# Kernel optimization log

Hardware: AMD Instinct MI355X
Metric: run time of the kernel (lower is better)

The kernel has to match this reference:

```python
import jax, jax.numpy as jnp
import numpy as np

N = 100000   # nodes
E = 1600000  # edges (edge_index1)
F_IN = 53    # num_features_xd
D1 = 128     # output_dim1
D2 = 64      # output_dim2
G = 512      # graphs in batch


def setup_inputs() -> dict:
    key = jax.random.key(0)
    ks = jax.random.split(key, 16)
    kaiming = lambda k, fi, fo: jax.random.normal(k, (fi, fo), jnp.float32) * np.float32(np.sqrt(2.0 / fi))
    glorot = lambda k, fi, fo: jax.random.normal(k, (fi, fo), jnp.float32) * np.float32(np.sqrt(1.0 / fi))
    return {
        "x": jax.random.normal(ks[0], (N, F_IN), jnp.float32),
        "edge_inter": jax.random.randint(ks[1], (2, E), 0, N),
        "edge_intra": jax.random.randint(ks[2], (2, E), 0, N),
        "batch": jnp.sort(jax.random.randint(ks[3], (N,), 0, G)),
        "num_graphs": G,
        "w1": kaiming(ks[4], F_IN, D1), "b1": jnp.zeros((D1,), jnp.float32),
        "w2": kaiming(ks[5], D1, D2), "b2": jnp.zeros((D2,), jnp.float32),
        "gat_w": glorot(ks[6], D2, D2),
        "att_src": jax.random.normal(ks[7], (D2,), jnp.float32) * 0.1,
        "att_dst": jax.random.normal(ks[8], (D2,), jnp.float32) * 0.1,
        "gat_b": jnp.zeros((D2,), jnp.float32),
        "gcn_w": glorot(ks[9], D2, 2 * D2), "gcn_b": jnp.zeros((2 * D2,), jnp.float32),
        "fc1_w": glorot(ks[10], 2 * D2, 512), "fc1_b": jnp.zeros((512,), jnp.float32),
        "fc2_w": glorot(ks[11], 512, 256), "fc2_b": jnp.zeros((256,), jnp.float32),
        "out_w": glorot(ks[12], 256, 1), "out_b": jnp.zeros((1,), jnp.float32),
    }


def reference(x, edge_inter, edge_intra, batch, num_graphs,
              w1, b1, w2, b2, gat_w, att_src, att_dst, gat_b,
              gcn_w, gcn_b, fc1_w, fc1_b, fc2_w, fc2_b, out_w, out_b):
    n = x.shape[0]
    # node_embed: two dense layers + relu
    h = jax.nn.relu(x @ w1 + b1)
    h = jax.nn.relu(h @ w2 + b2)

    # add self-loops (PyG default for GATConv and GCNConv)
    loops = jnp.arange(n)
    src = jnp.concatenate([edge_inter[0], loops])  # message source j
    dst = jnp.concatenate([edge_inter[1], loops])  # message target i

    # ---- GATConv (heads=1): gather -> score -> edge softmax -> scatter ----
    hp = h @ gat_w                           # [N, D2]
    a_s = hp @ att_src                       # [N]
    a_d = hp @ att_dst                       # [N]
    e = jax.nn.leaky_relu(a_s[src] + a_d[dst], negative_slope=0.2)  # [E+N]
    emax = jax.ops.segment_max(e, dst, num_segments=n)
    ee = jnp.exp(e - emax[dst])
    denom = jax.ops.segment_sum(ee, dst, num_segments=n)
    alpha = ee / denom[dst]                  # edge softmax per target node
    h = jax.ops.segment_sum(alpha[:, None] * hp[src], dst, num_segments=n) + gat_b
    h = jax.nn.relu(h)

    # ---- GCNConv: symmetric-normalized sparse aggregation ----
    hw = h @ gcn_w                           # [N, 2*D2]
    deg = jax.ops.segment_sum(jnp.ones_like(e), dst, num_segments=n)
    d_inv = jnp.where(deg > 0, deg ** -0.5, 0.0)
    norm = d_inv[src] * d_inv[dst]           # [E+N]
    h = jax.ops.segment_sum(norm[:, None] * hw[src], dst, num_segments=n) + gcn_b
    h = jax.nn.relu(h)

    # ---- global max pool over graphs ----
    g = jax.ops.segment_max(h, batch, num_segments=num_graphs)
    g = jnp.maximum(g, 0.0)  # guard empty segments (-inf); h >= 0 after relu

    # ---- MLP head (dropout is identity in eval mode) ----
    z = jax.nn.relu(g @ fc1_w + fc1_b)
    z = jax.nn.relu(z @ fc2_w + fc2_b)
    return z @ out_w + out_b
```

## Files before the change

kernel.cpp:

```cpp
#include <hip/hip_runtime.h>
#include <hip/hip_bf16.h>

#define F_IN 53
#define D1   128
#define D2   64
#define D3   128
#define H1SZ 512
#define H2SZ 256

#define BUKSZ   256
#define BUKMAX  512
#define CAP     5120
#define PART_CH 4096

__global__ void k_vecproj(const float* __restrict__ gat_w,
                          const float* __restrict__ att_src,
                          const float* __restrict__ att_dst,
                          float* __restrict__ v_src, float* __restrict__ v_dst) {
    int k = threadIdx.x;
    float as = 0.f, ad = 0.f;
    #pragma unroll
    for (int c = 0; c < D2; ++c) {
        float w = gat_w[k * D2 + c];
        as = fmaf(w, att_src[c], as);
        ad = fmaf(w, att_dst[c], ad);
    }
    v_src[k] = as;
    v_dst[k] = ad;
}

__global__ __launch_bounds__(256) void k_fused(const float* __restrict__ x,
                                               const float* __restrict__ w1,
                                               const float* __restrict__ b1,
                                               const float* __restrict__ w2,
                                               const float* __restrict__ b2,
                                               const float* __restrict__ gat_w,
                                               const float* __restrict__ v_src,
                                               const float* __restrict__ v_dst,
                                               float* __restrict__ hp,
                                               float* __restrict__ a_s,
                                               float* __restrict__ a_d,
                                               const int* __restrict__ ei,
                                               int* __restrict__ gcount,
                                               int2* __restrict__ tmp,
                                               const int* __restrict__ batch,
                                               int* __restrict__ gstart,
                                               int N, int E, int NBUK, int G,
                                               int embB, int partB) {
    __shared__ __align__(16) union {
        struct { float buf[32][64]; float h1s[32][D1]; } e;
        int hist[BUKMAX];
    } sm;
    int tid = threadIdx.x;
    int bid = blockIdx.x;

    if (bid >= embB) {
        if (bid < embB + partB) {
            for (int i = tid; i < NBUK; i += 256) sm.hist[i] = 0;
            __syncthreads();
            int k0 = (bid - embB) * PART_CH;
            int ss[16], dd[16];
            #pragma unroll
            for (int i = 0; i < 16; ++i) {
                int k = k0 + i * 256 + tid;
                if (k < E) {
                    ss[i] = ei[k];
                    dd[i] = ei[E + k];
                    atomicAdd(&sm.hist[dd[i] >> 8], 1);
                } else {
                    dd[i] = -1;
                }
            }
            __syncthreads();
            for (int b = tid; b < NBUK; b += 256) {
                int c = sm.hist[b];
                if (c > 0) sm.hist[b] = b * CAP + atomicAdd(&gcount[b], c);
            }
            __syncthreads();
            #pragma unroll
            for (int i = 0; i < 16; ++i) {
                if (dd[i] >= 0) {
                    int b = dd[i] >> 8;
                    int pos = atomicAdd(&sm.hist[b], 1);
                    if (pos < (b + 1) * CAP) tmp[pos] = make_int2(ss[i], dd[i]);
                }
            }
        } else {
            int n = (bid - embB - partB) * 256 + tid;
            if (n < N) {
                int b = batch[n];
                if (n == 0) {
                    for (int g = 0; g <= b; ++g) gstart[g] = 0;
                } else {
                    int pb = batch[n - 1];
                    for (int g = pb + 1; g <= b; ++g) gstart[g] = n;
                }
                if (n == N - 1) {
                    for (int g = b + 1; g <= G; ++g) gstart[g] = N;
                }
            }
        }
        return;
    }

    int n0 = bid * 32;
    for (int i = tid; i < 32 * F_IN; i += 256) {
        int node = i / F_IN, kk = i - node * F_IN;
        sm.e.buf[node][kk] = x[(size_t)n0 * F_IN + i];
    }
    __syncthreads();
    int c = tid & 63, grp = tid >> 6;
    int nb = grp * 8;
    {
        float acc0[8], acc1[8];
        float bb0 = b1[c], bb1 = b1[c + 64];
        #pragma unroll
        for (int j = 0; j < 8; ++j) { acc0[j] = bb0; acc1[j] = bb1; }
        #pragma unroll 1
        for (int kc = 0; kc < 13; ++kc) {
            int k4 = kc * 4;
            float wa0 = w1[(k4 + 0) * D1 + c];
            float wa1 = w1[(k4 + 1) * D1 + c];
            float wa2 = w1[(k4 + 2) * D1 + c];
            float wa3 = w1[(k4 + 3) * D1 + c];
            float wb0 = w1[(k4 + 0) * D1 + c + 64];
            float wb1 = w1[(k4 + 1) * D1 + c + 64];
            float wb2 = w1[(k4 + 2) * D1 + c + 64];
            float wb3 = w1[(k4 + 3) * D1 + c + 64];
            #pragma unroll
            for (int j = 0; j < 8; ++j) {
                float4 xv = *reinterpret_cast<const float4*>(&sm.e.buf[nb + j][k4]);
                acc0[j] = fmaf(xv.x, wa0, acc0[j]);
                acc0[j] = fmaf(xv.y, wa1, acc0[j]);
                acc0[j] = fmaf(xv.z, wa2, acc0[j]);
                acc0[j] = fmaf(xv.w, wa3, acc0[j]);
                acc1[j] = fmaf(xv.x, wb0, acc1[j]);
                acc1[j] = fmaf(xv.y, wb1, acc1[j]);
                acc1[j] = fmaf(xv.z, wb2, acc1[j]);
                acc1[j] = fmaf(xv.w, wb3, acc1[j]);
            }
        }
        {
            float wa = w1[52 * D1 + c], wb = w1[52 * D1 + c + 64];
            #pragma unroll
            for (int j = 0; j < 8; ++j) {
                float xv = sm.e.buf[nb + j][52];
                acc0[j] = fmaf(xv, wa, acc0[j]);
                acc1[j] = fmaf(xv, wb, acc1[j]);
            }
        }
        #pragma unroll
        for (int j = 0; j < 8; ++j) {
            sm.e.h1s[nb + j][c]      = fmaxf(acc0[j], 0.f);
            sm.e.h1s[nb + j][c + 64] = fmaxf(acc1[j], 0.f);
        }
    }
    float h2v[8];
    {
        float bb = b2[c];
        #pragma unroll
        for (int j = 0; j < 8; ++j) h2v[j] = bb;
        #pragma unroll 1
        for (int kc = 0; kc < 32; ++kc) {
            int k4 = kc * 4;
            float w0 = w2[(k4 + 0) * D2 + c];
            float w1v = w2[(k4 + 1) * D2 + c];
            float w2v = w2[(k4 + 2) * D2 + c];
            float w3v = w2[(k4 + 3) * D2 + c];
            #pragma unroll
            for (int j = 0; j < 8; ++j) {
                float4 hv = *reinterpret_cast<const float4*>(&sm.e.h1s[nb + j][k4]);
                h2v[j] = fmaf(hv.x, w0, h2v[j]);
                h2v[j] = fmaf(hv.y, w1v, h2v[j]);
                h2v[j] = fmaf(hv.z, w2v, h2v[j]);
                h2v[j] = fmaf(hv.w, w3v, h2v[j]);
            }
        }
        #pragma unroll
        for (int j = 0; j < 8; ++j) {
            float v = fmaxf(h2v[j], 0.f);
            h2v[j] = v;
            sm.e.buf[nb + j][c] = v;
        }
    }
    {
        float vs = v_src[c], vd = v_dst[c];
        #pragma unroll
        for (int j = 0; j < 8; ++j) {
            float ps = h2v[j] * vs, pd = h2v[j] * vd;
            #pragma unroll
            for (int off = 32; off; off >>= 1) {
                ps += __shfl_down(ps, off);
                pd += __shfl_down(pd, off);
            }
            if (c == 0) { int n = n0 + nb + j; a_s[n] = ps; a_d[n] = pd; }
        }
    }
    {
        float acc[8];
        #pragma unroll
        for (int j = 0; j < 8; ++j) acc[j] = 0.f;
        #pragma unroll 1
        for (int kc = 0; kc < 16; ++kc) {
            int k4 = kc * 4;
            float w0 = gat_w[(k4 + 0) * D2 + c];
            float w1v = gat_w[(k4 + 1) * D2 + c];
            float w2v = gat_w[(k4 + 2) * D2 + c];
            float w3v = gat_w[(k4 + 3) * D2 + c];
            #pragma unroll
            for (int j = 0; j < 8; ++j) {
                float4 hv = *reinterpret_cast<const float4*>(&sm.e.buf[nb + j][k4]);
                acc[j] = fmaf(hv.x, w0, acc[j]);
                acc[j] = fmaf(hv.y, w1v, acc[j]);
                acc[j] = fmaf(hv.z, w2v, acc[j]);
                acc[j] = fmaf(hv.w, w3v, acc[j]);
            }
        }
        #pragma unroll
        for (int j = 0; j < 8; ++j)
            hp[(size_t)(n0 + nb + j) * D2 + c] = acc[j];
    }
}

__global__ __launch_bounds__(256) void k_build(const int2* __restrict__ tmp,
                                               const int* __restrict__ gcount,
                                               int* __restrict__ offs,
                                               int* __restrict__ degi,
                                               float* __restrict__ dinv,
                                               int* __restrict__ csr_src, int N) {
    __shared__ int ldeg[256];
    __shared__ int lsc[256];
    __shared__ int lcur[256];
    __shared__ int pref[256];
    int tid = threadIdx.x;
    int b = blockIdx.x;
    int n0 = b * BUKSZ;
    int nvalid = min(BUKSZ, N - n0);
    int cnt = min(gcount[b], CAP);
    int acc = 0;
    for (int i = tid; i < b; i += 256) acc += min(gcount[i], CAP);
    pref[tid] = acc;
    ldeg[tid] = 0;
    __syncthreads();
    #pragma unroll
    for (int off = 128; off; off >>= 1) {
        if (tid < off) pref[tid] += pref[tid + off];
        __syncthreads();
    }
    int base = pref[0] + n0;
    for (int i = tid; i < cnt; i += 256) {
        int2 e = tmp[b * CAP + i];
        atomicAdd(&ldeg[e.y & 255], 1);
    }
    __syncthreads();
    int d = (tid < nvalid) ? (ldeg[tid] + 1) : 0;
    lsc[tid] = d;
    __syncthreads();
    #pragma unroll
    for (int off = 1; off < 256; off <<= 1) {
        int u = (tid >= off) ? lsc[tid - off] : 0;
        __syncthreads();
        lsc[tid] += u;
        __syncthreads();
    }
    int excl = lsc[tid] - d;
    if (tid < nvalid) {
        int n = n0 + tid;
        offs[n] = base + excl;
        degi[n] = d;
        dinv[n] = rsqrtf((float)d);
        lcur[tid] = excl;
    }
    __syncthreads();
    for (int i = tid; i < cnt; i += 256) {
        int2 e = tmp[b * CAP + i];
        int nl = e.y & 255;
        int r = atomicAdd(&lcur[nl], 1);
        csr_src[base + r] = e.x;
    }
    __syncthreads();
    if (tid < nvalid) {
        int r = atomicAdd(&lcur[tid], 1);
        csr_src[base + r] = n0 + tid;
    }
}

__global__ __launch_bounds__(256) void k_gat(const int* __restrict__ csr_src,
                                             const int* __restrict__ offs,
                                             const int* __restrict__ degi,
                                             const float* __restrict__ a_s,
                                             const float* __restrict__ a_d,
                                             const float* __restrict__ hp,
                                             const float* __restrict__ gat_b,
                                             const float* __restrict__ dinv,
                                             float* __restrict__ hscaled, int N) {
    __shared__ float ac[4][128];
    __shared__ int   si[4][128];
    int wv = threadIdx.x >> 6, lane = threadIdx.x & 63;
    int node = blockIdx.x * 4 + wv;
    if (node >= N) return;
    int start = offs[node], deg = degi[node];
    int dcap = min(deg, 128);
    float adn = a_d[node];
    float m = -1e30f, ssum = 0.f;
    for (int p = lane; p < deg; p += 64) {
        int s = csr_src[start + p];
        float e = a_s[s] + adn;
        e = (e > 0.f) ? e : 0.2f * e;
        if (p < 128) { ac[wv][p] = e; si[wv][p] = s; }
        float mn = fmaxf(m, e);
        ssum = ssum * __expf(m - mn) + __expf(e - mn);
        m = mn;
    }
    #pragma unroll
    for (int off = 32; off; off >>= 1) {
        float om = __shfl_xor(m, off);
        float os = __shfl_xor(ssum, off);
        float mn = fmaxf(m, om);
        ssum = ssum * __expf(m - mn) + os * __expf(om - mn);
        m = mn;
    }
    float rinv = 1.0f / ssum;
    if (lane < dcap)      ac[wv][lane]      = __expf(ac[wv][lane] - m) * rinv;
    if (lane + 64 < dcap) ac[wv][lane + 64] = __expf(ac[wv][lane + 64] - m) * rinv;
    float acc = 0.f;
    for (int pp = 0; pp < dcap; pp += 16) {
        int s[16]; float w[16];
        #pragma unroll
        for (int i = 0; i < 16; ++i) {
            int q = pp + i;
            int qc = (q < dcap) ? q : (dcap - 1);
            s[i] = si[wv][qc];
            w[i] = (q < dcap) ? ac[wv][q] : 0.f;
        }
        float v[16];
        #pragma unroll
        for (int i = 0; i < 16; ++i) v[i] = hp[(size_t)s[i] * D2 + lane];
        #pragma unroll
        for (int i = 0; i < 16; ++i) acc = fmaf(w[i], v[i], acc);
    }
    for (int p = 128; p < deg; ++p) {
        int s = csr_src[start + p];
        float e = a_s[s] + adn;
        e = (e > 0.f) ? e : 0.2f * e;
        acc = fmaf(__expf(e - m) * rinv, hp[(size_t)s * D2 + lane], acc);
    }
    hscaled[(size_t)node * D2 + lane] = dinv[node] * fmaxf(acc + gat_b[lane], 0.f);
}

__global__ __launch_bounds__(256) void k_gcn(const int* __restrict__ csr_src,
                                             const int* __restrict__ offs,
                                             const int* __restrict__ degi,
                                             const float* __restrict__ dinv,
                                             const float* __restrict__ hscaled,
                                             float* __restrict__ hagg, int N) {
    int node = blockIdx.x * 4 + (threadIdx.x >> 6);
    int lane = threadIdx.x & 63;
    if (node >= N) return;
    int start = offs[node], deg = degi[node];
    float acc = 0.f;
    for (int pp = 0; pp < deg; pp += 16) {
        int s[16];
        #pragma unroll
        for (int i = 0; i < 16; ++i) {
            int q = pp + i;
            int qc = (q < deg) ? q : (deg - 1);
            s[i] = csr_src[start + qc];
        }
        float v[16];
        #pragma unroll
        for (int i = 0; i < 16; ++i) v[i] = hscaled[(size_t)s[i] * D2 + lane];
        #pragma unroll
        for (int i = 0; i < 16; ++i) acc += (pp + i < deg) ? v[i] : 0.f;
    }
    hagg[(size_t)node * D2 + lane] = acc * dinv[node];
}

__global__ __launch_bounds__(512) void k_pool(const float* __restrict__ hagg,
                                              const float* __restrict__ gcn_w,
                                              const float* __restrict__ gcn_b,
                                              const int* __restrict__ gstart,
                                              float* __restrict__ g) {
    __shared__ float ws[D2 * D3];
    __shared__ __align__(16) float rows[16 * D2];
    __shared__ float red[512];
    int tid = threadIdx.x;
    int gi = blockIdx.x;
    for (int i = tid; i < D2 * D3; i += 512) ws[i] = gcn_w[i];
    int ns = gstart[gi], ne = gstart[gi + 1];
    int col = tid & 127, grp = tid >> 7;
    float bias = gcn_b[col];
    float runmax = 0.f;
    for (int base = ns; base < ne; base += 16) {
        int cnt = min(16, ne - base);
        __syncthreads();
        for (int i = tid; i < cnt * D2; i += 512)
            rows[i] = hagg[(size_t)base * D2 + i];
        __syncthreads();
        int nb = grp * 4;
        float a0 = bias, a1 = bias, a2 = bias, a3 = bias;
        #pragma unroll 4
        for (int kc = 0; kc < 16; ++kc) {
            int k4 = kc * 4;
            float w0 = ws[(k4 + 0) * D3 + col];
            float w1v = ws[(k4 + 1) * D3 + col];
            float w2v = ws[(k4 + 2) * D3 + col];
            float w3v = ws[(k4 + 3) * D3 + col];
            float4 r0 = *reinterpret_cast<const float4*>(&rows[(nb + 0) * D2 + k4]);
            float4 r1 = *reinterpret_cast<const float4*>(&rows[(nb + 1) * D2 + k4]);
            float4 r2 = *reinterpret_cast<const float4*>(&rows[(nb + 2) * D2 + k4]);
            float4 r3 = *reinterpret_cast<const float4*>(&rows[(nb + 3) * D2 + k4]);
            a0 = fmaf(r0.x, w0, a0); a0 = fmaf(r0.y, w1v, a0);
            a0 = fmaf(r0.z, w2v, a0); a0 = fmaf(r0.w, w3v, a0);
            a1 = fmaf(r1.x, w0, a1); a1 = fmaf(r1.y, w1v, a1);
            a1 = fmaf(r1.z, w2v, a1); a1 = fmaf(r1.w, w3v, a1);
            a2 = fmaf(r2.x, w0, a2); a2 = fmaf(r2.y, w1v, a2);
            a2 = fmaf(r2.z, w2v, a2); a2 = fmaf(r2.w, w3v, a2);
            a3 = fmaf(r3.x, w0, a3); a3 = fmaf(r3.y, w1v, a3);
            a3 = fmaf(r3.z, w2v, a3); a3 = fmaf(r3.w, w3v, a3);
        }
        if (nb + 0 < cnt) runmax = fmaxf(runmax, a0);
        if (nb + 1 < cnt) runmax = fmaxf(runmax, a1);
        if (nb + 2 < cnt) runmax = fmaxf(runmax, a2);
        if (nb + 3 < cnt) runmax = fmaxf(runmax, a3);
    }
    red[tid] = runmax;
    __syncthreads();
    if (tid < 128) {
        float v = fmaxf(fmaxf(red[tid], red[tid + 128]),
                        fmaxf(red[tid + 256], red[tid + 384]));
        g[(size_t)gi * D3 + tid] = v;
    }
}

__global__ __launch_bounds__(512) void k_fc1(const float* __restrict__ g,
                                             const float* __restrict__ w,
                                             const float* __restrict__ b,
                                             float* __restrict__ z1) {
    __shared__ float gs[4 * D3];
    int t = threadIdx.x;
    int g0 = blockIdx.x * 4;
    if (t < 4 * D3) gs[t] = g[(size_t)g0 * D3 + t];
    __syncthreads();
    float bias = b[t];
    float a0 = bias, a1 = bias, a2 = bias, a3 = bias;
    for (int k = 0; k < D3; ++k) {
        float wv = w[k * H1SZ + t];
        a0 = fmaf(gs[k], wv, a0);
        a1 = fmaf(gs[D3 + k], wv, a1);
        a2 = fmaf(gs[2 * D3 + k], wv, a2);
        a3 = fmaf(gs[3 * D3 + k], wv, a3);
    }
    z1[(size_t)(g0 + 0) * H1SZ + t] = fmaxf(a0, 0.f);
    z1[(size_t)(g0 + 1) * H1SZ + t] = fmaxf(a1, 0.f);
    z1[(size_t)(g0 + 2) * H1SZ + t] = fmaxf(a2, 0.f);
    z1[(size_t)(g0 + 3) * H1SZ + t] = fmaxf(a3, 0.f);
}

__global__ __launch_bounds__(256) void k_fc2(const float* __restrict__ z1,
                                             const float* __restrict__ w,
                                             const float* __restrict__ b,
                                             float* __restrict__ z2) {
    __shared__ float zs[4 * H1SZ];
    int t = threadIdx.x;
    int g0 = blockIdx.x * 4;
    for (int i = t; i < 4 * H1SZ; i += 256) zs[i] = z1[(size_t)g0 * H1SZ + i];
    __syncthreads();
    float bias = b[t];
    float a0 = bias, a1 = bias, a2 = bias, a3 = bias;
    for (int k = 0; k < H1SZ; ++k) {
        float wv = w[k * H2SZ + t];
        a0 = fmaf(zs[k], wv, a0);
        a1 = fmaf(zs[H1SZ + k], wv, a1);
        a2 = fmaf(zs[2 * H1SZ + k], wv, a2);
        a3 = fmaf(zs[3 * H1SZ + k], wv, a3);
    }
    z2[(size_t)(g0 + 0) * H2SZ + t] = fmaxf(a0, 0.f);
    z2[(size_t)(g0 + 1) * H2SZ + t] = fmaxf(a1, 0.f);
    z2[(size_t)(g0 + 2) * H2SZ + t] = fmaxf(a2, 0.f);
    z2[(size_t)(g0 + 3) * H2SZ + t] = fmaxf(a3, 0.f);
}

__global__ __launch_bounds__(256) void k_out(const float* __restrict__ z2,
                                             const float* __restrict__ out_w,
                                             const float* __restrict__ out_b,
                                             float* __restrict__ out) {
    __shared__ float red[4];
    int gi = blockIdx.x, t = threadIdx.x;
    float p = z2[(size_t)gi * H2SZ + t] * out_w[t];
    #pragma unroll
    for (int off = 32; off; off >>= 1) p += __shfl_down(p, off);
    int lane = t & 63, w = t >> 6;
    if (lane == 0) red[w] = p;
    __syncthreads();
    if (t == 0) out[gi] = red[0] + red[1] + red[2] + red[3] + out_b[0];
}

extern "C" void kernel_launch(void* const* d_in, const int* in_sizes, int n_in,
                              void* d_out, int out_size, void* d_ws, size_t ws_size,
                              hipStream_t stream) {
    const float* x        = (const float*)d_in[0];
    const int*   ei       = (const int*)d_in[1];
    const int*   batch    = (const int*)d_in[3];
    const float* w1       = (const float*)d_in[5];
    const float* b1       = (const float*)d_in[6];
    const float* w2       = (const float*)d_in[7];
    const float* b2       = (const float*)d_in[8];
    const float* gat_w    = (const float*)d_in[9];
    const float* att_src  = (const float*)d_in[10];
    const float* att_dst  = (const float*)d_in[11];
    const float* gat_b    = (const float*)d_in[12];
    const float* gcn_w    = (const float*)d_in[13];
    const float* gcn_b    = (const float*)d_in[14];
    const float* fc1_w    = (const float*)d_in[15];
    const float* fc1_b    = (const float*)d_in[16];
    const float* fc2_w    = (const float*)d_in[17];
    const float* fc2_b    = (const float*)d_in[18];
    const float* out_w    = (const float*)d_in[19];
    const float* out_b    = (const float*)d_in[20];
    float* out = (float*)d_out;

    const int N = in_sizes[0] / F_IN;
    const int E = in_sizes[1] / 2;
    const int M = E + N;
    const int G = out_size;
    const int NBUK = (N + BUKSZ - 1) / BUKSZ;
    const int embB   = N / 32;
    const int partB  = (E + PART_CH - 1) / PART_CH;
    const int boundB = (N + 255) / 256;

    char* p = (char*)d_ws;
    size_t off = 0;
    auto alloc = [&](size_t bytes) { void* q = p + off; off += (bytes + 255) & ~(size_t)255; return q; };
    int2*  tmp     = (int2*)alloc((size_t)NBUK * CAP * 8);
    int*   csr_src = (int*)alloc((size_t)M * 4);
    float* hp      = (float*)alloc((size_t)N * D2 * 4);
    float* hscaled = (float*)alloc((size_t)N * D2 * 4);
    float* hagg    = (float*)alloc((size_t)N * D2 * 4);
    int*   offs    = (int*)alloc((size_t)N * 4);
    int*   degi    = (int*)alloc((size_t)N * 4);
    float* dinv    = (float*)alloc((size_t)N * 4);
    float* a_s     = (float*)alloc((size_t)N * 4);
    float* a_d     = (float*)alloc((size_t)N * 4);
    int*   gcount  = (int*)alloc((size_t)NBUK * 4);
    int*   gstart  = (int*)alloc((size_t)(G + 1) * 4);
    float* g       = (float*)alloc((size_t)G * D3 * 4);
    float* z1      = (float*)alloc((size_t)G * H1SZ * 4);
    float* z2      = (float*)alloc((size_t)G * H2SZ * 4);
    float* v_src   = (float*)alloc(D2 * 4);
    float* v_dst   = (float*)alloc(D2 * 4);

    hipMemsetAsync(gcount, 0, (size_t)NBUK * 4, stream);

    k_vecproj<<<1, 64, 0, stream>>>(gat_w, att_src, att_dst, v_src, v_dst);
    k_fused<<<embB + partB + boundB, 256, 0, stream>>>(
        x, w1, b1, w2, b2, gat_w, v_src, v_dst, hp, a_s, a_d,
        ei, gcount, tmp, batch, gstart, N, E, NBUK, G, embB, partB);
    k_build<<<NBUK, 256, 0, stream>>>(tmp, gcount, offs, degi, dinv, csr_src, N);
    k_gat<<<(N + 3) / 4, 256, 0, stream>>>(csr_src, offs, degi, a_s, a_d, hp,
                                           gat_b, dinv, hscaled, N);
    k_gcn<<<(N + 3) / 4, 256, 0, stream>>>(csr_src, offs, degi, dinv, hscaled, hagg, N);
    k_pool<<<G, 512, 0, stream>>>(hagg, gcn_w, gcn_b, gstart, g);
    k_fc1<<<G / 4, 512, 0, stream>>>(g, fc1_w, fc1_b, z1);
    k_fc2<<<G / 4, 256, 0, stream>>>(z1, fc2_w, fc2_b, z2);
    k_out<<<G, 256, 0, stream>>>(z2, out_w, out_b, out);
}
```

Before: 349.9 us.

## Fuse MLP head into one kernel and read x directly in embed layer

The three MLP-head kernels (fc1, fc2, output) become a single kernel that keeps the intermediates in shared memory. This removes two launches and the global round trips for z1 and z2. Separately, the first embedding layer no longer stages x in LDS. It reads x rows straight from global memory with a wave-uniform base (readfirstlane), so each scalar load is broadcast across the wave. That drops a shared-memory copy and a barrier, at the cost of many small, unvectorized global reads and losing the float4 LDS reads.

Result: slower. 370.4 us (+5.8%).

```diff
diff --git a/kernel.cpp b/kernel.cpp
--- a/kernel.cpp
+++ b/kernel.cpp
@@ -104,49 +104,23 @@
     }
 
     int n0 = bid * 32;
-    for (int i = tid; i < 32 * F_IN; i += 256) {
-        int node = i / F_IN, kk = i - node * F_IN;
-        sm.e.buf[node][kk] = x[(size_t)n0 * F_IN + i];
-    }
-    __syncthreads();
     int c = tid & 63, grp = tid >> 6;
-    int nb = grp * 8;
+    int nb = __builtin_amdgcn_readfirstlane(grp * 8);
     {
         float acc0[8], acc1[8];
         float bb0 = b1[c], bb1 = b1[c + 64];
         #pragma unroll
         for (int j = 0; j < 8; ++j) { acc0[j] = bb0; acc1[j] = bb1; }
+        const float* xr = x + (size_t)(n0 + nb) * F_IN;
         #pragma unroll 1
-        for (int kc = 0; kc < 13; ++kc) {
-            int k4 = kc * 4;
-            float wa0 = w1[(k4 + 0) * D1 + c];
-            float wa1 = w1[(k4 + 1) * D1 + c];
-            float wa2 = w1[(k4 + 2) * D1 + c];
-            float wa3 = w1[(k4 + 3) * D1 + c];
-            float wb0 = w1[(k4 + 0) * D1 + c + 64];
-            float wb1 = w1[(k4 + 1) * D1 + c + 64];
-            float wb2 = w1[(k4 + 2) * D1 + c + 64];
-            float wb3 = w1[(k4 + 3) * D1 + c + 64];
+        for (int k = 0; k < F_IN; ++k) {
+            float wA = w1[k * D1 + c];
+            float wB = w1[k * D1 + c + 64];
             #pragma unroll
             for (int j = 0; j < 8; ++j) {
-                float4 xv = *reinterpret_cast<const float4*>(&sm.e.buf[nb + j][k4]);
-                acc0[j] = fmaf(xv.x, wa0, acc0[j]);
-                acc0[j] = fmaf(xv.y, wa1, acc0[j]);
-                acc0[j] = fmaf(xv.z, wa2, acc0[j]);
-                acc0[j] = fmaf(xv.w, wa3, acc0[j]);
-                acc1[j] = fmaf(xv.x, wb0, acc1[j]);
-                acc1[j] = fmaf(xv.y, wb1, acc1[j]);
-                acc1[j] = fmaf(xv.z, wb2, acc1[j]);
-                acc1[j] = fmaf(xv.w, wb3, acc1[j]);
-            }
-        }
-        {
-            float wa = w1[52 * D1 + c], wb = w1[52 * D1 + c + 64];
-            #pragma unroll
-            for (int j = 0; j < 8; ++j) {
-                float xv = sm.e.buf[nb + j][52];
-                acc0[j] = fmaf(xv, wa, acc0[j]);
-                acc1[j] = fmaf(xv, wb, acc1[j]);
+                float xv = xr[j * F_IN + k];
+                acc0[j] = fmaf(xv, wA, acc0[j]);
+                acc1[j] = fmaf(xv, wB, acc1[j]);
             }
         }
         #pragma unroll
@@ -433,67 +407,64 @@
     }
 }
 
-__global__ __launch_bounds__(512) void k_fc1(const float* __restrict__ g,
-                                             const float* __restrict__ w,
-                                             const float* __restrict__ b,
-                                             float* __restrict__ z1) {
+__global__ __launch_bounds__(512) void k_mlp(const float* __restrict__ g,
+                                             const float* __restrict__ fc1_w,
+                                             const float* __restrict__ fc1_b,
+                                             const float* __restrict__ fc2_w,
+                                             const float* __restrict__ fc2_b,
+                                             const float* __restrict__ out_w,
+                                             const float* __restrict__ out_b,
+                                             float* __restrict__ out) {
     __shared__ float gs[4 * D3];
+    __shared__ float zs[4 * H1SZ];
+    __shared__ float z2s[4 * H2SZ];
+    __shared__ float red[8];
     int t = threadIdx.x;
     int g0 = blockIdx.x * 4;
     if (t < 4 * D3) gs[t] = g[(size_t)g0 * D3 + t];
     __syncthreads();
-    float bias = b[t];
-    float a0 = bias, a1 = bias, a2 = bias, a3 = bias;
-    for (int k = 0; k < D3; ++k) {
-        float wv = w[k * H1SZ + t];
-        a0 = fmaf(gs[k], wv, a0);
-        a1 = fmaf(gs[D3 + k], wv, a1);
-        a2 = fmaf(gs[2 * D3 + k], wv, a2);
-        a3 = fmaf(gs[3 * D3 + k], wv, a3);
-    }
-    z1[(size_t)(g0 + 0) * H1SZ + t] = fmaxf(a0, 0.f);
-    z1[(size_t)(g0 + 1) * H1SZ + t] = fmaxf(a1, 0.f);
-    z1[(size_t)(g0 + 2) * H1SZ + t] = fmaxf(a2, 0.f);
-    z1[(size_t)(g0 + 3) * H1SZ + t] = fmaxf(a3, 0.f);
-}
-
-__global__ __launch_bounds__(256) void k_fc2(const float* __restrict__ z1,
-                                             const float* __restrict__ w,
-                                             const float* __restrict__ b,
-                                             float* __restrict__ z2) {
-    __shared__ float zs[4 * H1SZ];
-    int t = threadIdx.x;
-    int g0 = blockIdx.x * 4;
-    for (int i = t; i < 4 * H1SZ; i += 256) zs[i] = z1[(size_t)g0 * H1SZ + i];
-    __syncthreads();
-    float bias = b[t];
-    float a0 = bias, a1 = bias, a2 = bias, a3 = bias;
-    for (int k = 0; k < H1SZ; ++k) {
-        float wv = w[k * H2SZ + t];
-        a0 = fmaf(zs[k], wv, a0);
-        a1 = fmaf(zs[H1SZ + k], wv, a1);
-        a2 = fmaf(zs[2 * H1SZ + k], wv, a2);
-        a3 = fmaf(zs[3 * H1SZ + k], wv, a3);
-    }
-    z2[(size_t)(g0 + 0) * H2SZ + t] = fmaxf(a0, 0.f);
-    z2[(size_t)(g0 + 1) * H2SZ + t] = fmaxf(a1, 0.f);
-    z2[(size_t)(g0 + 2) * H2SZ + t] = fmaxf(a2, 0.f);
-    z2[(size_t)(g0 + 3) * H2SZ + t] = fmaxf(a3, 0.f);
-}
-
-__global__ __launch_bounds__(256) void k_out(const float* __restrict__ z2,
-                                             const float* __restrict__ out_w,
-                                             const float* __restrict__ out_b,
-                                             float* __restrict__ out) {
-    __shared__ float red[4];
-    int gi = blockIdx.x, t = threadIdx.x;
-    float p = z2[(size_t)gi * H2SZ + t] * out_w[t];
-    #pragma unroll
-    for (int off = 32; off; off >>= 1) p += __shfl_down(p, off);
-    int lane = t & 63, w = t >> 6;
-    if (lane == 0) red[w] = p;
-    __syncthreads();
-    if (t == 0) out[gi] = red[0] + red[1] + red[2] + red[3] + out_b[0];
+    {
+        float bias = fc1_b[t];
+        float a0 = bias, a1 = bias, a2 = bias, a3 = bias;
+        for (int k = 0; k < D3; ++k) {
+            float wv = fc1_w[k * H1SZ + t];
+            a0 = fmaf(gs[k], wv, a0);
+            a1 = fmaf(gs[D3 + k], wv, a1);
+            a2 = fmaf(gs[2 * D3 + k], wv, a2);
+            a3 = fmaf(gs[3 * D3 + k], wv, a3);
+        }
+        zs[0 * H1SZ + t] = fmaxf(a0, 0.f);
+        zs[1 * H1SZ + t] = fmaxf(a1, 0.f);
+        zs[2 * H1SZ + t] = fmaxf(a2, 0.f);
+        zs[3 * H1SZ + t] = fmaxf(a3, 0.f);
+    }
+    __syncthreads();
+    {
+        int ct = t & 255, jp = t >> 8;
+        float bias = fc2_b[ct];
+        float a0 = bias, a1 = bias;
+        const float* zA = &zs[(2 * jp) * H1SZ];
+        const float* zB = &zs[(2 * jp + 1) * H1SZ];
+        for (int k = 0; k < H1SZ; ++k) {
+            float wv = fc2_w[k * H2SZ + ct];
+            a0 = fmaf(zA[k], wv, a0);
+            a1 = fmaf(zB[k], wv, a1);
+        }
+        z2s[(2 * jp) * H2SZ + ct] = fmaxf(a0, 0.f);
+        z2s[(2 * jp + 1) * H2SZ + ct] = fmaxf(a1, 0.f);
+    }
+    __syncthreads();
+    {
+        int j = t >> 7, c2 = t & 127;
+        float p = z2s[j * H2SZ + c2] * out_w[c2]
+                + z2s[j * H2SZ + c2 + 128] * out_w[c2 + 128];
+        #pragma unroll
+        for (int off = 32; off; off >>= 1) p += __shfl_down(p, off);
+        int lane = t & 63, w8 = t >> 6;
+        if (lane == 0) red[w8] = p;
+        __syncthreads();
+        if (t < 4) out[g0 + t] = red[2 * t] + red[2 * t + 1] + out_b[0];
+    }
 }
 
 extern "C" void kernel_launch(void* const* d_in, const int* in_sizes, int n_in,
@@ -545,8 +516,6 @@
     int*   gcount  = (int*)alloc((size_t)NBUK * 4);
     int*   gstart  = (int*)alloc((size_t)(G + 1) * 4);
     float* g       = (float*)alloc((size_t)G * D3 * 4);
-    float* z1      = (float*)alloc((size_t)G * H1SZ * 4);
-    float* z2      = (float*)alloc((size_t)G * H2SZ * 4);
     float* v_src   = (float*)alloc(D2 * 4);
     float* v_dst   = (float*)alloc(D2 * 4);
 
@@ -561,7 +530,5 @@
                                            gat_b, dinv, hscaled, N);
     k_gcn<<<(N + 3) / 4, 256, 0, stream>>>(csr_src, offs, degi, dinv, hscaled, hagg, N);
     k_pool<<<G, 512, 0, stream>>>(hagg, gcn_w, gcn_b, gstart, g);
-    k_fc1<<<G / 4, 512, 0, stream>>>(g, fc1_w, fc1_b, z1);
-    k_fc2<<<G / 4, 256, 0, stream>>>(z1, fc2_w, fc2_b, z2);
-    k_out<<<G, 256, 0, stream>>>(z2, out_w, out_b, out);
-}
+    k_mlp<<<G / 4, 512, 0, stream>>>(g, fc1_w, fc1_b, fc2_w, fc2_b, out_w, out_b, out);
+}
```
